# Kernel tuning notes

Hardware: AMD Instinct MI355X
Metric: run time of the kernel (lower is better)

Reference implementation:

```python
import jax, jax.numpy as jnp
import numpy as np

DIM = 512
NUM_HEADS = 8
HEAD_DIM = DIM // NUM_HEADS
SCALE = HEAD_DIM ** -0.5


def setup_inputs() -> dict:
    key = jax.random.key(0)
    k_x, k_qkv, k_proj, k_pb = jax.random.split(key, 4)
    x = jax.random.normal(k_x, (2, 4096, DIM), dtype=jnp.float32)
    # nn.Linear weights: stored as [out, in]; qkv_bias=False so no qkv bias.
    w_qkv = jax.random.normal(k_qkv, (3 * DIM, DIM), dtype=jnp.float32) * (DIM ** -0.5)
    w_proj = jax.random.normal(k_proj, (DIM, DIM), dtype=jnp.float32) * (DIM ** -0.5)
    b_proj = jax.random.normal(k_pb, (DIM,), dtype=jnp.float32) * 0.01
    return {"x": x, "w_qkv": w_qkv, "w_proj": w_proj, "b_proj": b_proj}


def reference(x, w_qkv, w_proj, b_proj):
    B, N, D = x.shape
    H, Hd = NUM_HEADS, HEAD_DIM
    # qkv: [B, N, 3D] -> [3, B, H, N, Hd]
    qkv = (x @ w_qkv.T).reshape(B, N, 3, H, Hd).transpose(2, 0, 3, 1, 4)
    q, k, v = qkv[0], qkv[1], qkv[2]
    # Naive full attention matrix in fp32 (matches original non-fused path).
    attn = jnp.einsum('bhqd,bhkd->bhqk', q, k) * SCALE
    attn = jax.nn.softmax(attn, axis=-1)
    out = jnp.einsum('bhqk,bhkd->bhqd', attn, v)
    out = out.transpose(0, 2, 1, 3).reshape(B, N, D)
    return out @ w_proj.T + b_proj
```

## Files before the change

kernel.cpp:

```cpp
#include <hip/hip_runtime.h>
#include <stdint.h>

#define SEQ   4096
#define DIMM  512
#define HDIM  64
#define NH    8
#define ROWS  8192
#define QKVN  1536

typedef __attribute__((ext_vector_type(8))) __bf16 bf16x8;
typedef __attribute__((ext_vector_type(4))) float  f32x4;
typedef __attribute__((ext_vector_type(2))) uint32_t u32x2;

__device__ __forceinline__ uint16_t f2bfu(float f) {
  uint32_t u = __builtin_bit_cast(uint32_t, f);
  return (uint16_t)((u + 0x7FFFu + ((u >> 16) & 1u)) >> 16);
}

__device__ __forceinline__ f32x4 mfma16(bf16x8 a, bf16x8 b, f32x4 c) {
  return __builtin_amdgcn_mfma_f32_16x16x32_bf16(a, b, c, 0, 0, 0);
}

#if __has_builtin(__builtin_amdgcn_exp2f)
#define EXP2F(x) __builtin_amdgcn_exp2f(x)
#else
#define EXP2F(x) exp2f(x)
#endif

__device__ __forceinline__ void gld16(const void* g, void* l) {
  __builtin_amdgcn_global_load_lds(
      (const __attribute__((address_space(1))) uint32_t*)g,
      (__attribute__((address_space(3))) uint32_t*)l, 16, 0, 0);
}

#define X4  (ROWS * DIMM / 4)
#define Q4  (QKVN * DIMM / 4)
#define P4  (DIMM * DIMM / 4)

__global__ __launch_bounds__(256) void cvt_kernel(
    const float* __restrict__ x, const float* __restrict__ wq,
    const float* __restrict__ wp, uint16_t* __restrict__ xb,
    uint16_t* __restrict__ wqb, uint16_t* __restrict__ wpb) {
  int idx = blockIdx.x * 256 + threadIdx.x;
  const float* src; uint16_t* dst; int i4;
  if (idx < X4)            { src = x;  dst = xb;  i4 = idx; }
  else if (idx < X4 + Q4)  { src = wq; dst = wqb; i4 = idx - X4; }
  else                     { src = wp; dst = wpb; i4 = idx - X4 - Q4; }
  float4 v = ((const float4*)src)[i4];
  ushort4 o;
  o.x = f2bfu(v.x); o.y = f2bfu(v.y); o.z = f2bfu(v.z); o.w = f2bfu(v.w);
  ((ushort4*)dst)[i4] = o;
}

__device__ __forceinline__ void gemm_core(
    const uint16_t* __restrict__ A, const uint16_t* __restrict__ B,
    uint16_t* As, uint16_t* Bs, f32x4 acc[4][4]) {
  const int tid = threadIdx.x;
  const int lane = tid & 63, wave = tid >> 6;
  const int quad = lane >> 4, l16 = lane & 15;
  const int wr = (wave & 1) * 64, wc = (wave >> 1) * 64;
  const int bm = blockIdx.x, bn = blockIdx.y;
  const int sw = (l16 >> 1) & 3;

  for (int kt = 0; kt < DIMM / 32; ++kt) {
#pragma unroll
    for (int it = 0; it < 2; ++it) {
      int L = it * 256 + tid;
      int r = L >> 2, c = L & 3;
      int gc = c ^ ((r >> 1) & 3);
      int ldsoff = (it * 256 + (tid & ~63)) * 16;
      gld16((const char*)A + ((size_t)(bm * 128 + r) * DIMM + kt * 32) * 2 + gc * 16,
            (char*)As + ldsoff);
      gld16((const char*)B + ((size_t)(bn * 128 + r) * DIMM + kt * 32) * 2 + gc * 16,
            (char*)Bs + ldsoff);
    }
    __syncthreads();
    bf16x8 af[4], bfr[4];
#pragma unroll
    for (int i = 0; i < 4; ++i)
      af[i] = *(const bf16x8*)(As + (wr + i * 16 + l16) * 32 + ((quad ^ sw) * 8));
#pragma unroll
    for (int j = 0; j < 4; ++j)
      bfr[j] = *(const bf16x8*)(Bs + (wc + j * 16 + l16) * 32 + ((quad ^ sw) * 8));
#pragma unroll
    for (int i = 0; i < 4; ++i)
#pragma unroll
      for (int j = 0; j < 4; ++j)
        acc[i][j] = mfma16(af[i], bfr[j], acc[i][j]);
    __syncthreads();
  }
}

__global__ __launch_bounds__(256, 2) void qkv_gemm(
    const uint16_t* __restrict__ xb, const uint16_t* __restrict__ wqb,
    uint16_t* __restrict__ qd, uint16_t* __restrict__ kd,
    uint16_t* __restrict__ vt) {
  __shared__ __align__(16) uint16_t As[128 * 32];
  __shared__ __align__(16) uint16_t Bs[128 * 32];
  f32x4 acc[4][4];
#pragma unroll
  for (int i = 0; i < 4; ++i)
#pragma unroll
    for (int j = 0; j < 4; ++j) acc[i][j] = f32x4{0.f, 0.f, 0.f, 0.f};

  gemm_core(xb, wqb, As, Bs, acc);

  const int lane = threadIdx.x & 63, wave = threadIdx.x >> 6;
  const int quad = lane >> 4, l16 = lane & 15;
  const int wr = (wave & 1) * 64, wc = (wave >> 1) * 64;
  const float qscale = 0.125f * 1.44269504f;
#pragma unroll
  for (int i = 0; i < 4; ++i) {
    int m0 = blockIdx.x * 128 + wr + i * 16 + quad * 4;
    int b = m0 >> 12, n0 = m0 & 4095;
#pragma unroll
    for (int j = 0; j < 4; ++j) {
      int jc = blockIdx.y * 128 + wc + j * 16 + l16;
      int region = jc >> 9;
      int h = (jc >> 6) & 7, hd = jc & 63;
      int bh = (b << 3) | h;
      if (region == 0) {
#pragma unroll
        for (int r = 0; r < 4; ++r)
          qd[((size_t)bh * SEQ + n0 + r) * HDIM + hd] = f2bfu(acc[i][j][r] * qscale);
      } else if (region == 1) {
#pragma unroll
        for (int r = 0; r < 4; ++r)
          kd[((size_t)bh * SEQ + n0 + r) * HDIM + hd] = f2bfu(acc[i][j][r]);
      } else {
        ushort4 pk;
        pk.x = f2bfu(acc[i][j][0]); pk.y = f2bfu(acc[i][j][1]);
        pk.z = f2bfu(acc[i][j][2]); pk.w = f2bfu(acc[i][j][3]);
        *(ushort4*)(vt + ((size_t)bh * HDIM + hd) * SEQ + n0) = pk;
      }
    }
  }
}

__global__ __launch_bounds__(512, 4) void attn_kernel(
    const uint16_t* __restrict__ qd, const uint16_t* __restrict__ kd,
    const uint16_t* __restrict__ vt, uint16_t* __restrict__ ao) {
  __shared__ __align__(16) uint16_t Ks[128 * 64];
  __shared__ __align__(16) uint16_t Vs[64 * 128];
  __shared__ __align__(16) uint16_t Ps[8][32 * 64];

  const int tid = threadIdx.x, lane = tid & 63, wave = tid >> 6;
  const int quad = lane >> 4, l16 = lane & 15;
  const int pair = wave >> 1, khalf = wave & 1;
  const int qt = blockIdx.x, bh = blockIdx.y;
  const size_t base_qk = (size_t)bh * SEQ * HDIM;
  const size_t base_v  = (size_t)bh * HDIM * SEQ;
  const int sw7 = l16 & 7;
  char* Pw = (char*)Ps + wave * 4096;

  bf16x8 qf[2][2];
#pragma unroll
  for (int it2 = 0; it2 < 2; ++it2)
#pragma unroll
    for (int kh = 0; kh < 2; ++kh)
      qf[it2][kh] = *(const bf16x8*)(qd + base_qk +
          (size_t)(qt * 128 + pair * 32 + it2 * 16 + l16) * HDIM + kh * 32 + quad * 8);

  f32x4 O[2][4];
  float lsum[2] = {0.f, 0.f};
#pragma unroll
  for (int a = 0; a < 2; ++a)
#pragma unroll
    for (int d = 0; d < 4; ++d) O[a][d] = f32x4{0.f, 0.f, 0.f, 0.f};

  for (int kt = 0; kt < SEQ / 128; ++kt) {
#pragma unroll
    for (int it = 0; it < 2; ++it) {
      int L = it * 512 + tid;
      int ldsoff = (it * 512 + (tid & ~63)) * 16;
      int rk = L >> 3, ck = L & 7;
      int gck = ck ^ (rk & 7);
      gld16((const char*)kd + (base_qk + (size_t)(kt * 128 + rk) * HDIM) * 2 + gck * 16,
            (char*)Ks + ldsoff);
      int rv = L >> 4, cv = L & 15;
      int gcv = cv ^ (rv & 15);
      gld16((const char*)vt + (base_v + (size_t)rv * SEQ + (size_t)kt * 128) * 2 + gcv * 16,
            (char*)Vs + ldsoff);
    }
    __syncthreads();

    f32x4 P[4][2];
#pragma unroll
    for (int jh = 0; jh < 4; ++jh) {
      int jf = khalf * 4 + jh;
      const uint16_t* krow = Ks + (jf * 16 + l16) * 64;
      bf16x8 kf0 = *(const bf16x8*)(krow + ((quad ^ sw7) * 8));
      bf16x8 kf1 = *(const bf16x8*)(krow + (((4 + quad) ^ sw7) * 8));
#pragma unroll
      for (int it2 = 0; it2 < 2; ++it2) {
        f32x4 s = f32x4{0.f, 0.f, 0.f, 0.f};
        s = mfma16(kf0, qf[it2][0], s);
        s = mfma16(kf1, qf[it2][1], s);
        P[jh][it2] = s;
      }
    }

#pragma unroll
    for (int jh = 0; jh < 4; ++jh)
#pragma unroll
      for (int it2 = 0; it2 < 2; ++it2) {
        float p0 = EXP2F(P[jh][it2][0]);
        float p1 = EXP2F(P[jh][it2][1]);
        float p2 = EXP2F(P[jh][it2][2]);
        float p3 = EXP2F(P[jh][it2][3]);
        lsum[it2] += (p0 + p1) + (p2 + p3);
        uint32_t a0 = __builtin_bit_cast(uint32_t, p0) + 0x8000u;
        uint32_t a1 = __builtin_bit_cast(uint32_t, p1) + 0x8000u;
        uint32_t a2 = __builtin_bit_cast(uint32_t, p2) + 0x8000u;
        uint32_t a3 = __builtin_bit_cast(uint32_t, p3) + 0x8000u;
        u32x2 pk;
        pk.x = (a0 >> 16) | (a1 & 0xFFFF0000u);
        pk.y = (a2 >> 16) | (a3 & 0xFFFF0000u);
        int c16 = (jh * 2 + (quad >> 1)) ^ sw7;
        *(u32x2*)(Pw + (it2 * 16 + l16) * 128 + c16 * 16 + (quad & 1) * 8) = pk;
      }

#pragma unroll
    for (int kp = 0; kp < 2; ++kp) {
      bf16x8 pb[2];
#pragma unroll
      for (int it2 = 0; it2 < 2; ++it2)
        pb[it2] = *(const bf16x8*)(Pw + (it2 * 16 + l16) * 128 +
                                   (((kp * 4 + quad) ^ sw7) * 16));
      bf16x8 va[4];
#pragma unroll
      for (int dl = 0; dl < 4; ++dl)
        va[dl] = *(const bf16x8*)((const char*)Vs + (dl * 16 + l16) * 256 +
                                  (((khalf * 8 + kp * 4 + quad) ^ l16) & 15) * 16);
#pragma unroll
      for (int it2 = 0; it2 < 2; ++it2)
#pragma unroll
        for (int dl = 0; dl < 4; ++dl)
          O[it2][dl] = mfma16(va[dl], pb[it2], O[it2][dl]);
    }
    __syncthreads();
  }

  if (!(wave & 1)) {
    f32x4* ob = (f32x4*)((char*)Ps + wave * 4096);
#pragma unroll
    for (int it2 = 0; it2 < 2; ++it2)
#pragma unroll
      for (int dl = 0; dl < 4; ++dl)
        ob[(it2 * 4 + dl) * 64 + lane] = O[it2][dl];
    float2* lb = (float2*)((char*)Ks + pair * 512);
    lb[lane] = make_float2(lsum[0], lsum[1]);
  }
  __syncthreads();
  if (wave & 1) {
    const f32x4* ob = (const f32x4*)((char*)Ps + (wave - 1) * 4096);
    float2 lp = ((const float2*)((char*)Ks + pair * 512))[lane];
    lsum[0] += lp.x; lsum[1] += lp.y;
#pragma unroll
    for (int it2 = 0; it2 < 2; ++it2)
#pragma unroll
      for (int dl = 0; dl < 4; ++dl)
        O[it2][dl] += ob[(it2 * 4 + dl) * 64 + lane];

    const int b = bh >> 3, h = bh & 7;
#pragma unroll
    for (int it2 = 0; it2 < 2; ++it2) {
      float l = lsum[it2];
      l += __shfl_xor(l, 16);
      l += __shfl_xor(l, 32);
      float inv = 1.0f / l;
      int q = qt * 128 + pair * 32 + it2 * 16 + l16;
      size_t rowbase = ((size_t)(b * SEQ + q)) * DIMM + h * HDIM;
#pragma unroll
      for (int dl = 0; dl < 4; ++dl) {
        ushort4 pk;
        pk.x = f2bfu(O[it2][dl][0] * inv);
        pk.y = f2bfu(O[it2][dl][1] * inv);
        pk.z = f2bfu(O[it2][dl][2] * inv);
        pk.w = f2bfu(O[it2][dl][3] * inv);
        *(ushort4*)(ao + rowbase + dl * 16 + quad * 4) = pk;
      }
    }
  }
}

__global__ __launch_bounds__(256, 2) void proj_gemm(
    const uint16_t* __restrict__ ao, const uint16_t* __restrict__ wpb,
    const float* __restrict__ bprj, float* __restrict__ out) {
  __shared__ __align__(16) uint16_t As[128 * 32];
  __shared__ __align__(16) uint16_t Bs[128 * 32];
  f32x4 acc[4][4];
#pragma unroll
  for (int i = 0; i < 4; ++i)
#pragma unroll
    for (int j = 0; j < 4; ++j) acc[i][j] = f32x4{0.f, 0.f, 0.f, 0.f};

  gemm_core(ao, wpb, As, Bs, acc);

  const int lane = threadIdx.x & 63, wave = threadIdx.x >> 6;
  const int quad = lane >> 4, l16 = lane & 15;
  const int wr = (wave & 1) * 64, wc = (wave >> 1) * 64;
#pragma unroll
  for (int i = 0; i < 4; ++i) {
    int m0 = blockIdx.x * 128 + wr + i * 16 + quad * 4;
#pragma unroll
    for (int j = 0; j < 4; ++j) {
      int jc = blockIdx.y * 128 + wc + j * 16 + l16;
      float bias = bprj[jc];
#pragma unroll
      for (int r = 0; r < 4; ++r)
        out[(size_t)(m0 + r) * DIMM + jc] = acc[i][j][r] + bias;
    }
  }
}

extern "C" void kernel_launch(void* const* d_in, const int* in_sizes, int n_in,
                              void* d_out, int out_size, void* d_ws, size_t ws_size,
                              hipStream_t stream) {
  const float* x     = (const float*)d_in[0];
  const float* wqkv  = (const float*)d_in[1];
  const float* wproj = (const float*)d_in[2];
  const float* bproj = (const float*)d_in[3];

  char* ws = (char*)d_ws;
  uint16_t* xb  = (uint16_t*)(ws + 0);
  uint16_t* wqb = (uint16_t*)(ws + 8388608);
  uint16_t* wpb = (uint16_t*)(ws + 9961472);
  uint16_t* qd  = (uint16_t*)(ws + 10485760);
  uint16_t* kd  = (uint16_t*)(ws + 18874368);
  uint16_t* vt  = (uint16_t*)(ws + 27262976);
  uint16_t* ao  = (uint16_t*)(ws + 35651584);

  cvt_kernel<<<(X4 + Q4 + P4) / 256, 256, 0, stream>>>(x, wqkv, wproj, xb, wqb, wpb);
  qkv_gemm<<<dim3(64, 12), 256, 0, stream>>>(xb, wqb, qd, kd, vt);
  attn_kernel<<<dim3(32, 16), 512, 0, stream>>>(qd, kd, vt, ao);
  proj_gemm<<<dim3(64, 4), 256, 0, stream>>>(ao, wpb, bproj, (float*)d_out);
}
```

Before: 191.8 us.

## Use hardware bf16 pack conversion, XCD-aware attention block mapping, and MFMA priority hints

Replaces the software round-to-nearest bf16 conversion with the v_cvt_pk_bf16_f32 instruction throughout all kernels, packing two values per instruction. The attention grid is flattened and remapped so each XCD handles a fixed pair of heads, which improves K/V reuse in each XCD's L2. Separately, K fragments are loaded before the QK MFMA loop, and the MFMA sections are wrapped in s_setprio hints to favor matrix issue across waves. The inline asm depends on the target supporting this instruction, and the block remapping assumes round-robin dispatch of blocks across 8 XCDs.

```diff
diff --git a/kernel.cpp b/kernel.cpp
--- a/kernel.cpp
+++ b/kernel.cpp
@@ -12,9 +12,10 @@
 typedef __attribute__((ext_vector_type(4))) float  f32x4;
 typedef __attribute__((ext_vector_type(2))) uint32_t u32x2;
 
-__device__ __forceinline__ uint16_t f2bfu(float f) {
-  uint32_t u = __builtin_bit_cast(uint32_t, f);
-  return (uint16_t)((u + 0x7FFFu + ((u >> 16) & 1u)) >> 16);
+__device__ __forceinline__ uint32_t cvtpk(float lo, float hi) {
+  uint32_t w;
+  asm("v_cvt_pk_bf16_f32 %0, %1, %2" : "=v"(w) : "v"(lo), "v"(hi));
+  return w;
 }
 
 __device__ __forceinline__ f32x4 mfma16(bf16x8 a, bf16x8 b, f32x4 c) {
@@ -47,9 +48,10 @@
   else if (idx < X4 + Q4)  { src = wq; dst = wqb; i4 = idx - X4; }
   else                     { src = wp; dst = wpb; i4 = idx - X4 - Q4; }
   float4 v = ((const float4*)src)[i4];
-  ushort4 o;
-  o.x = f2bfu(v.x); o.y = f2bfu(v.y); o.z = f2bfu(v.z); o.w = f2bfu(v.w);
-  ((ushort4*)dst)[i4] = o;
+  uint2 o;
+  o.x = cvtpk(v.x, v.y);
+  o.y = cvtpk(v.z, v.w);
+  ((uint2*)dst)[i4] = o;
 }
 
 __device__ __forceinline__ void gemm_core(
@@ -120,18 +122,26 @@
       int h = (jc >> 6) & 7, hd = jc & 63;
       int bh = (b << 3) | h;
       if (region == 0) {
-#pragma unroll
-        for (int r = 0; r < 4; ++r)
-          qd[((size_t)bh * SEQ + n0 + r) * HDIM + hd] = f2bfu(acc[i][j][r] * qscale);
+        uint32_t w01 = cvtpk(acc[i][j][0] * qscale, acc[i][j][1] * qscale);
+        uint32_t w23 = cvtpk(acc[i][j][2] * qscale, acc[i][j][3] * qscale);
+        size_t rb = ((size_t)bh * SEQ + n0) * HDIM + hd;
+        qd[rb]            = (uint16_t)w01;
+        qd[rb + HDIM]     = (uint16_t)(w01 >> 16);
+        qd[rb + 2 * HDIM] = (uint16_t)w23;
+        qd[rb + 3 * HDIM] = (uint16_t)(w23 >> 16);
       } else if (region == 1) {
-#pragma unroll
-        for (int r = 0; r < 4; ++r)
-          kd[((size_t)bh * SEQ + n0 + r) * HDIM + hd] = f2bfu(acc[i][j][r]);
+        uint32_t w01 = cvtpk(acc[i][j][0], acc[i][j][1]);
+        uint32_t w23 = cvtpk(acc[i][j][2], acc[i][j][3]);
+        size_t rb = ((size_t)bh * SEQ + n0) * HDIM + hd;
+        kd[rb]            = (uint16_t)w01;
+        kd[rb + HDIM]     = (uint16_t)(w01 >> 16);
+        kd[rb + 2 * HDIM] = (uint16_t)w23;
+        kd[rb + 3 * HDIM] = (uint16_t)(w23 >> 16);
       } else {
-        ushort4 pk;
-        pk.x = f2bfu(acc[i][j][0]); pk.y = f2bfu(acc[i][j][1]);
-        pk.z = f2bfu(acc[i][j][2]); pk.w = f2bfu(acc[i][j][3]);
-        *(ushort4*)(vt + ((size_t)bh * HDIM + hd) * SEQ + n0) = pk;
+        uint2 pk;
+        pk.x = cvtpk(acc[i][j][0], acc[i][j][1]);
+        pk.y = cvtpk(acc[i][j][2], acc[i][j][3]);
+        *(uint2*)(vt + ((size_t)bh * HDIM + hd) * SEQ + n0) = pk;
       }
     }
   }
@@ -147,7 +157,10 @@
   const int tid = threadIdx.x, lane = tid & 63, wave = tid >> 6;
   const int quad = lane >> 4, l16 = lane & 15;
   const int pair = wave >> 1, khalf = wave & 1;
-  const int qt = blockIdx.x, bh = blockIdx.y;
+  const int wid = blockIdx.x;
+  const int xcd = wid & 7, slot = wid >> 3;
+  const int bh = xcd + 8 * (slot & 1);
+  const int qt = slot >> 1;
   const size_t base_qk = (size_t)bh * SEQ * HDIM;
   const size_t base_v  = (size_t)bh * HDIM * SEQ;
   const int sw7 = l16 & 7;
@@ -184,21 +197,26 @@
     }
     __syncthreads();
 
-    f32x4 P[4][2];
+    bf16x8 kf[4][2];
 #pragma unroll
     for (int jh = 0; jh < 4; ++jh) {
       int jf = khalf * 4 + jh;
       const uint16_t* krow = Ks + (jf * 16 + l16) * 64;
-      bf16x8 kf0 = *(const bf16x8*)(krow + ((quad ^ sw7) * 8));
-      bf16x8 kf1 = *(const bf16x8*)(krow + (((4 + quad) ^ sw7) * 8));
+      kf[jh][0] = *(const bf16x8*)(krow + ((quad ^ sw7) * 8));
+      kf[jh][1] = *(const bf16x8*)(krow + (((4 + quad) ^ sw7) * 8));
+    }
+    f32x4 P[4][2];
+    __builtin_amdgcn_s_setprio(1);
+#pragma unroll
+    for (int jh = 0; jh < 4; ++jh)
 #pragma unroll
       for (int it2 = 0; it2 < 2; ++it2) {
         f32x4 s = f32x4{0.f, 0.f, 0.f, 0.f};
-        s = mfma16(kf0, qf[it2][0], s);
-        s = mfma16(kf1, qf[it2][1], s);
+        s = mfma16(kf[jh][0], qf[it2][0], s);
+        s = mfma16(kf[jh][1], qf[it2][1], s);
         P[jh][it2] = s;
       }
-    }
+    __builtin_amdgcn_s_setprio(0);
 
 #pragma unroll
     for (int jh = 0; jh < 4; ++jh)
@@ -209,13 +227,9 @@
         float p2 = EXP2F(P[jh][it2][2]);
         float p3 = EXP2F(P[jh][it2][3]);
         lsum[it2] += (p0 + p1) + (p2 + p3);
-        uint32_t a0 = __builtin_bit_cast(uint32_t, p0) + 0x8000u;
-        uint32_t a1 = __builtin_bit_cast(uint32_t, p1) + 0x8000u;
-        uint32_t a2 = __builtin_bit_cast(uint32_t, p2) + 0x8000u;
-        uint32_t a3 = __builtin_bit_cast(uint32_t, p3) + 0x8000u;
         u32x2 pk;
-        pk.x = (a0 >> 16) | (a1 & 0xFFFF0000u);
-        pk.y = (a2 >> 16) | (a3 & 0xFFFF0000u);
+        pk.x = cvtpk(p0, p1);
+        pk.y = cvtpk(p2, p3);
         int c16 = (jh * 2 + (quad >> 1)) ^ sw7;
         *(u32x2*)(Pw + (it2 * 16 + l16) * 128 + c16 * 16 + (quad & 1) * 8) = pk;
       }
@@ -232,11 +246,13 @@
       for (int dl = 0; dl < 4; ++dl)
         va[dl] = *(const bf16x8*)((const char*)Vs + (dl * 16 + l16) * 256 +
                                   (((khalf * 8 + kp * 4 + quad) ^ l16) & 15) * 16);
+      __builtin_amdgcn_s_setprio(1);
 #pragma unroll
       for (int it2 = 0; it2 < 2; ++it2)
 #pragma unroll
         for (int dl = 0; dl < 4; ++dl)
           O[it2][dl] = mfma16(va[dl], pb[it2], O[it2][dl]);
+      __builtin_amdgcn_s_setprio(0);
     }
     __syncthreads();
   }
@@ -273,12 +289,10 @@
       size_t rowbase = ((size_t)(b * SEQ + q)) * DIMM + h * HDIM;
 #pragma unroll
       for (int dl = 0; dl < 4; ++dl) {
-        ushort4 pk;
-        pk.x = f2bfu(O[it2][dl][0] * inv);
-        pk.y = f2bfu(O[it2][dl][1] * inv);
-        pk.z = f2bfu(O[it2][dl][2] * inv);
-        pk.w = f2bfu(O[it2][dl][3] * inv);
-        *(ushort4*)(ao + rowbase + dl * 16 + quad * 4) = pk;
+        uint2 pk;
+        pk.x = cvtpk(O[it2][dl][0] * inv, O[it2][dl][1] * inv);
+        pk.y = cvtpk(O[it2][dl][2] * inv, O[it2][dl][3] * inv);
+        *(uint2*)(ao + rowbase + dl * 16 + quad * 4) = pk;
       }
     }
   }
@@ -333,6 +347,6 @@
 
   cvt_kernel<<<(X4 + Q4 + P4) / 256, 256, 0, stream>>>(x, wqkv, wproj, xb, wqb, wpb);
   qkv_gemm<<<dim3(64, 12), 256, 0, stream>>>(xb, wqb, qd, kd, vt);
-  attn_kernel<<<dim3(32, 16), 512, 0, stream>>>(qd, kd, vt, ao);
+  attn_kernel<<<512, 512, 0, stream>>>(qd, kd, vt, ao);
   proj_gemm<<<dim3(64, 4), 256, 0, stream>>>(ao, wpb, bproj, (float*)d_out);
 }
```

Result: faster. 183.2 us (-4.5%).
